# Performance work log

Measured on AMD Instinct MI355X. Metric: run time of the kernel, lower is better.

The kernel has to match this reference:

```python
import jax, jax.numpy as jnp
import numpy as np

B, N, DIM, HEADS = 2, 1024, 1024, 16
HD = DIM // HEADS  # 64


def setup_inputs() -> dict:
    key = jax.random.key(0)
    ks = jax.random.split(key, 8)
    f = lambda k, s: jax.random.normal(k, s, dtype=jnp.float32)
    inv = np.float32(1.0 / np.sqrt(DIM))
    return {
        'x_real': f(ks[0], (B, N, DIM)),
        'x_imag': f(ks[1], (B, N, DIM)),
        'freqs_real': f(ks[2], (N, HD)),
        'freqs_imag': f(ks[3], (N, HD)),
        'Wqkv_r': f(ks[4], (3 * DIM, DIM)) * inv,
        'Wqkv_i': f(ks[5], (3 * DIM, DIM)) * inv,
        'bqkv_r': jnp.zeros((3 * DIM,), jnp.float32),
        'bqkv_i': jnp.zeros((3 * DIM,), jnp.float32),
        'Wout_r': f(ks[6], (DIM, DIM)) * inv,
        'Wout_i': f(ks[7], (DIM, DIM)) * inv,
        'bout_r': jnp.zeros((DIM,), jnp.float32),
        'bout_i': jnp.zeros((DIM,), jnp.float32),
    }


def reference(x_real, x_imag, freqs_real, freqs_imag,
              Wqkv_r, Wqkv_i, bqkv_r, bqkv_i,
              Wout_r, Wout_i, bout_r, bout_i):
    cplx = jax.lax.complex
    x = cplx(x_real, x_imag)                    # [b, n, d] complex64
    Wqkv = cplx(Wqkv_r, Wqkv_i)                 # [3d, d]
    bqkv = cplx(bqkv_r, bqkv_i)
    Wout = cplx(Wout_r, Wout_i)
    bout = cplx(bout_r, bout_i)
    freqs = cplx(freqs_real, freqs_imag)        # [n, hd]

    scale = HD ** (-0.5)

    # ComplexLinear: x @ W^T + b -> [b, n, 3d]
    qkv = jnp.einsum('bnd,ed->bne', x, Wqkv) + bqkv
    # rearrange 'b n (h d qkv) -> qkv b h n d' (qkv index fastest-varying)
    qkv = qkv.reshape(B, N, HEADS, HD, 3)
    q = jnp.transpose(qkv[..., 0], (0, 2, 1, 3))  # [b, h, n, hd]
    k = jnp.transpose(qkv[..., 1], (0, 2, 1, 3))
    v = jnp.transpose(qkv[..., 2], (0, 2, 1, 3))

    # complex rotary: elementwise multiply by freqs [n, hd]
    q = q * freqs
    k = k * freqs

    # complex QK^H -> [b, h, n, n]
    dots = jnp.einsum('bhnd,bhmd->bhnm', q, jnp.conj(k))
    attn = jax.nn.softmax(jnp.abs(dots) * scale, axis=-1)  # real float32

    # real attn @ complex v (promotes to complex64)
    out = jnp.einsum('bhnm,bhmd->bhnd', attn, v)
    out = jnp.transpose(out, (0, 2, 1, 3)).reshape(B, N, DIM)  # b n (h d)

    out = jnp.einsum('bnd,ed->bne', out, Wout) + bout
    # return real/imag stacked so baseline comparison is on real arrays
    return jnp.stack([jnp.real(out), jnp.imag(out)], axis=0)  # [2, b, n, d]
```

## Files before the change

kernel.cpp:

```cpp
#include <hip/hip_runtime.h>
#include <hip/hip_bf16.h>
#include <stdint.h>

#define B 2
#define N 1024
#define DIM 1024
#define HEADS 16
#define HD 64
#define E3 (3*DIM)
#define M (B*N)

typedef __hip_bfloat16 bf16;
typedef __attribute__((ext_vector_type(8))) short short8v;
typedef __attribute__((ext_vector_type(4))) float f32x4;
typedef __attribute__((ext_vector_type(4))) unsigned int u32x4;

__device__ __forceinline__ float scrub(float v) {
    return (v == v && fabsf(v) < 1e30f) ? v : 0.0f;
}
__device__ __forceinline__ float b2f(bf16 x) { return scrub(__bfloat162float(x)); }

template<bool FP32>
__device__ __forceinline__ float ldin(const void* p, int i) {
    if (FP32) return scrub(((const float*)p)[i]);
    else      return scrub(__bfloat162float(((const bf16*)p)[i]));
}

__device__ __forceinline__ bool sniff_fp32(const void* x, int tid, int* sbad) {
    if (tid == 0) *sbad = 0;
    __syncthreads();
    if (tid < 64) {
        const unsigned short* u = (const unsigned short*)x;
        int ex = (u[tid] >> 7) & 0xFF;
        if (ex == 0xFF || ex >= 135 || (ex != 0 && ex <= 118))
            atomicAdd(sbad, 1);
    }
    __syncthreads();
    return *sbad > 4;
}

__device__ __forceinline__ short f2bs(float x) {
    bf16 h = __float2bfloat16(x);
    return __builtin_bit_cast(short, h);
}
__device__ __forceinline__ short8v neg8(short8v x) {
    u32x4 u = __builtin_bit_cast(u32x4, x);
    u ^= 0x80008000u;
    return __builtin_bit_cast(short8v, u);
}
__device__ __forceinline__ f32x4 mfma16(short8v a, short8v b, f32x4 c) {
    return __builtin_amdgcn_mfma_f32_16x16x32_bf16(a, b, c, 0, 0, 0);
}

__device__ __forceinline__ void cvt8(bf16* dhi, bf16* dlo, const float* s) {
    float4 a = *(const float4*)s;
    float4 b = *(const float4*)(s + 4);
    float v[8] = {a.x,a.y,a.z,a.w,b.x,b.y,b.z,b.w};
    short8v hi, lo;
    #pragma unroll
    for (int e = 0; e < 8; ++e) {
        float f = scrub(v[e]);
        bf16 h = __float2bfloat16(f);
        hi[e] = __builtin_bit_cast(short, h);
        lo[e] = f2bs(f - __bfloat162float(h));
    }
    *(short8v*)dhi = hi;
    *(short8v*)dlo = lo;
}
__device__ __forceinline__ void cvt8h(bf16* dhi, const float* s) {
    float4 a = *(const float4*)s;
    float4 b = *(const float4*)(s + 4);
    float v[8] = {a.x,a.y,a.z,a.w,b.x,b.y,b.z,b.w};
    short8v hi;
    #pragma unroll
    for (int e = 0; e < 8; ++e)
        hi[e] = f2bs(scrub(v[e]));
    *(short8v*)dhi = hi;
}

#define PLB 2048

__device__ __forceinline__ short8v frag_ldp(const bf16* base, int row, int j) {
    int p = row >> 1;
    int c = (((row & 1) << 2) | j) ^ (p & 7);
    return *(const short8v*)(base + p*64 + c*8);
}

template<int AMODE, int BMODE, int BM, int NI>
__device__ __forceinline__ void cgemm32(
    const void* Aor, const void* Aoi,
    const bf16* Arh, const bf16* Aih, const bf16* Arl, const bf16* Ail,
    const void* Bor, const void* Boi,
    const bf16* Brh, const bf16* Bih,
    int row0, int col0,
    bf16* sA, bf16* sB,
    f32x4 (*accr)[NI], f32x4 (*accs)[NI], f32x4 (*acci)[NI])
{
    constexpr bool ALO = (AMODE == 1 || AMODE == 2);
    constexpr bool BLO = (BMODE == 2);
    constexpr int  PLA = BM*32;

    const int t  = threadIdx.x;
    const int w  = t >> 6, l = t & 63;
    const int lr = l & 15, lg = l >> 4;
    const int wm = (NI == 4) ? w : (w >> 1);
    const int wn = (NI == 4) ? 0 : (w & 1);

    const int pb  = t >> 3;
    const int cpb = (t & 7) ^ (pb & 7);
    const int srb = 2*pb + (cpb >> 2);
    const int sjb = cpb & 3;

    for (int k0 = 0; k0 < DIM; k0 += 32) {
        #pragma unroll
        for (int u = 0; u < BM/64; ++u) {
            int c   = t + 256*u;
            int pa  = c >> 3;
            int cpa = (c & 7) ^ (pa & 7);
            int sra = 2*pa + (cpa >> 2);
            int sja = cpa & 3;
            size_t aoff = (size_t)(row0 + sra)*DIM + k0 + sja*8;
            bf16* dA = sA + c*8;
            if constexpr (AMODE == 0) {
                *(short8v*)(dA)        = *(const short8v*)((const bf16*)Aor + aoff);
                *(short8v*)(dA + PLA)  = *(const short8v*)((const bf16*)Aoi + aoff);
            } else if constexpr (AMODE == 1) {
                *(short8v*)(dA)         = *(const short8v*)(Arh + aoff);
                *(short8v*)(dA + PLA)   = *(const short8v*)(Aih + aoff);
                *(short8v*)(dA + 2*PLA) = *(const short8v*)(Arl + aoff);
                *(short8v*)(dA + 3*PLA) = *(const short8v*)(Ail + aoff);
            } else {
                cvt8(dA,       dA + 2*PLA, (const float*)Aor + aoff);
                cvt8(dA + PLA, dA + 3*PLA, (const float*)Aoi + aoff);
            }
        }
        {
            size_t boff = (size_t)(col0 + srb)*DIM + k0 + sjb*8;
            bf16* dB = sB + t*8;
            if constexpr (BMODE == 0) {
                *(short8v*)(dB)       = *(const short8v*)((const bf16*)Bor + boff);
                *(short8v*)(dB + PLB) = *(const short8v*)((const bf16*)Boi + boff);
            } else if constexpr (BMODE == 3) {
                *(short8v*)(dB)       = *(const short8v*)(Brh + boff);
                *(short8v*)(dB + PLB) = *(const short8v*)(Bih + boff);
            } else {
                cvt8(dB,       dB + 2*PLB, (const float*)Bor + boff);
                cvt8(dB + PLB, dB + 3*PLB, (const float*)Boi + boff);
            }
        }
        __syncthreads();

        short8v arh[2], aih[2], arl[2], ail[2];
        #pragma unroll
        for (int mi = 0; mi < 2; ++mi) {
            int arow = wm*32 + mi*16 + lr;
            arh[mi] = frag_ldp(sA,       arow, lg);
            aih[mi] = frag_ldp(sA + PLA, arow, lg);
            if constexpr (ALO) {
                arl[mi] = frag_ldp(sA + 2*PLA, arow, lg);
                ail[mi] = frag_ldp(sA + 3*PLA, arow, lg);
            }
        }
        #pragma unroll
        for (int ni = 0; ni < NI; ++ni) {
            int brow = wn*32 + ni*16 + lr;
            short8v brh = frag_ldp(sB,       brow, lg);
            short8v bih = frag_ldp(sB + PLB, brow, lg);
            short8v brl, bil;
            if constexpr (BLO) {
                brl = frag_ldp(sB + 2*PLB, brow, lg);
                bil = frag_ldp(sB + 3*PLB, brow, lg);
            }
            #pragma unroll
            for (int mi = 0; mi < 2; ++mi) {
                accr[mi][ni] = mfma16(arh[mi], brh, accr[mi][ni]);
                accs[mi][ni] = mfma16(aih[mi], bih, accs[mi][ni]);
                acci[mi][ni] = mfma16(arh[mi], bih, acci[mi][ni]);
                acci[mi][ni] = mfma16(aih[mi], brh, acci[mi][ni]);
                if constexpr (BLO) {
                    accr[mi][ni] = mfma16(arh[mi], brl, accr[mi][ni]);
                    accs[mi][ni] = mfma16(aih[mi], bil, accs[mi][ni]);
                    acci[mi][ni] = mfma16(arh[mi], bil, acci[mi][ni]);
                    acci[mi][ni] = mfma16(aih[mi], brl, acci[mi][ni]);
                }
                if constexpr (ALO) {
                    accr[mi][ni] = mfma16(arl[mi], brh, accr[mi][ni]);
                    accs[mi][ni] = mfma16(ail[mi], bih, accs[mi][ni]);
                    acci[mi][ni] = mfma16(arl[mi], bih, acci[mi][ni]);
                    acci[mi][ni] = mfma16(ail[mi], brh, acci[mi][ni]);
                }
            }
        }
        __syncthreads();
    }
}

struct PrepArgs {
    const void* src[6];
    bf16* hi[6];
    bf16* lo[6];
    int n8[6];
};

__global__ __launch_bounds__(256) void prepass_kernel(PrepArgs a) {
    __shared__ int sbad;
    const int y = blockIdx.y;
    bool f32 = sniff_fp32(a.src[y], threadIdx.x, &sbad);
    if (!f32) return;
    const int n8 = a.n8[y];
    bf16* lo = a.lo[y];
    for (int i = blockIdx.x*blockDim.x + threadIdx.x; i < n8; i += gridDim.x*blockDim.x) {
        if (lo) cvt8 (a.hi[y] + (size_t)i*8, lo + (size_t)i*8, (const float*)a.src[y] + (size_t)i*8);
        else    cvt8h(a.hi[y] + (size_t)i*8,                   (const float*)a.src[y] + (size_t)i*8);
    }
}

template<bool FP32>
__device__ __forceinline__ void qkv_epi(
    const void* fr_, const void* fi_, const void* bqr, const void* bqi,
    bf16* qr, bf16* qi, bf16* kr, bf16* ki, bf16* vr, bf16* vi,
    int row0, int col0,
    f32x4 (*accr)[4], f32x4 (*accs)[4], f32x4 (*acci)[4])
{
    const int t  = threadIdx.x;
    const int w  = t >> 6, l = t & 63;
    const int lr = l & 15, lg = l >> 4;

    #pragma unroll
    for (int ni = 0; ni < 4; ++ni) {
        int col = col0 + ni*16 + lr;
        float bre = ldin<FP32>(bqr, col);
        float bim = ldin<FP32>(bqi, col);
        int s = col % 3;
        int tc = col / 3;
        int h = tc / HD, d = tc % HD;
        #pragma unroll
        for (int mi = 0; mi < 2; ++mi)
        #pragma unroll
        for (int r = 0; r < 4; ++r) {
            int row = row0 + w*32 + mi*16 + 4*lg + r;
            int bb = row / N, n = row % N;
            float cr = accr[mi][ni][r] - accs[mi][ni][r] + bre;
            float ci = acci[mi][ni][r] + bim;
            if (s == 2) {
                int idxT = ((bb*HEADS + h)*HD + d)*N + n;
                vr[idxT] = __float2bfloat16(scrub(cr));
                vi[idxT] = __float2bfloat16(scrub(ci));
            } else {
                float fre = ldin<FP32>(fr_, n*HD + d);
                float fim = ldin<FP32>(fi_, n*HD + d);
                float rr = cr*fre - ci*fim;
                float ri = cr*fim + ci*fre;
                int idx = ((bb*HEADS + h)*N + n)*HD + d;
                if (s == 0) { qr[idx] = __float2bfloat16(scrub(rr)); qi[idx] = __float2bfloat16(scrub(ri)); }
                else        { kr[idx] = __float2bfloat16(scrub(rr)); ki[idx] = __float2bfloat16(scrub(ri)); }
            }
        }
    }
}

template<int FM>
__global__ __launch_bounds__(256, 3) void qkv_kernel(
    const void* xr, const void* xi, const void* fr_, const void* fi_,
    const void* Wr, const void* Wi, const void* bqr, const void* bqi,
    const bf16* xrh, const bf16* xih, const bf16* xrl, const bf16* xil,
    const bf16* wrh, const bf16* wih,
    bf16* qr, bf16* qi, bf16* kr, bf16* ki, bf16* vr, bf16* vi)
{
    __shared__ __align__(16) bf16 sA[4*128*32];
    __shared__ __align__(16) bf16 sB[(FM==1 ? 2 : 4)*PLB];
    __shared__ int sbad;
    bool f32 = sniff_fp32(xr, threadIdx.x, &sbad);

    int wg   = blockIdx.x;
    int xcd  = wg & 7;
    int idx  = wg >> 3;
    int ctl  = idx % 6;
    int rtg  = idx / 6;
    int row0 = rtg * 128;
    int col0 = (xcd*6 + ctl) * 64;

    f32x4 accr[2][4] = {}, accs[2][4] = {}, acci[2][4] = {};
    if (f32) {
        if constexpr (FM == 1)
            cgemm32<1, 3, 128, 4>(xr, xi, xrh, xih, xrl, xil,
                                  Wr, Wi, wrh, wih,
                                  row0, col0, sA, sB, accr, accs, acci);
        else
            cgemm32<2, 2, 128, 4>(xr, xi, nullptr, nullptr, nullptr, nullptr,
                                  Wr, Wi, nullptr, nullptr,
                                  row0, col0, sA, sB, accr, accs, acci);
        qkv_epi<true >(fr_, fi_, bqr, bqi, qr,qi,kr,ki,vr,vi, row0, col0, accr, accs, acci);
    } else {
        cgemm32<0, 0, 128, 4>(xr, xi, nullptr, nullptr, nullptr, nullptr,
                              Wr, Wi, nullptr, nullptr,
                              row0, col0, sA, sB, accr, accs, acci);
        qkv_epi<false>(fr_, fi_, bqr, bqi, qr,qi,kr,ki,vr,vi, row0, col0, accr, accs, acci);
    }
}

__device__ __forceinline__ short8v frag_ld(const bf16* base, int row, int j) {
    return *(const short8v*)(base + row*64 + ((j ^ (row & 7)) << 3));
}

__global__ __launch_bounds__(256) void attn_kernel(
    const bf16* qr, const bf16* qi, const bf16* kr, const bf16* ki,
    const bf16* vtr, const bf16* vti, bf16* aor_, bf16* aoi_)
{
    __shared__ __align__(16) bf16 skr[64*64];
    __shared__ __align__(16) bf16 ski[64*64];
    __shared__ __align__(16) bf16 svr[64*64];
    __shared__ __align__(16) bf16 svi[64*64];
    __shared__ __align__(16) bf16 sp[4][16*64];

    const int t  = threadIdx.x;
    const int w  = t >> 6;
    const int l  = t & 63;
    const int lr = l & 15;
    const int lg = l >> 4;
    int wg = blockIdx.x;
    int sw = (wg & 7) * ((int)gridDim.x >> 3) + (wg >> 3);
    const int qt = sw & 15;
    const int bh = sw >> 4;

    const size_t hbase = (size_t)bh * N * HD;

    const bf16* qrg = qr + hbase + (size_t)(qt*64 + w*16 + lr) * HD;
    const bf16* qig = qi + hbase + (size_t)(qt*64 + w*16 + lr) * HD;
    short8v qfr[2], qfi[2], qfrn[2];
    #pragma unroll
    for (int ks = 0; ks < 2; ++ks) {
        qfr[ks] = *(const short8v*)(qrg + 32*ks + 8*lg);
        qfi[ks] = *(const short8v*)(qig + 32*ks + 8*lg);
        qfrn[ks] = neg8(qfr[ks]);
    }

    const int cA = t, cB = t + 256;
    const int rA = cA >> 3, jA = (cA & 7) ^ (rA & 7);
    const int rB = cB >> 3, jB = (cB & 7) ^ (rB & 7);
    const bf16* krg = kr  + hbase;
    const bf16* kig = ki  + hbase;
    const bf16* vrg = vtr + hbase;
    const bf16* vig = vti + hbase;

    f32x4 outr[4], outi[4];
    #pragma unroll
    for (int dt = 0; dt < 4; ++dt) {
        outr[dt] = (f32x4){0.f,0.f,0.f,0.f};
        outi[dt] = (f32x4){0.f,0.f,0.f,0.f};
    }
    float mrow[4] = {-1e30f,-1e30f,-1e30f,-1e30f};
    float lrow[4] = {0.f,0.f,0.f,0.f};

    for (int kt = 0; kt < N/64; ++kt) {
        const int m0 = kt*64;
        *(short8v*)(skr + cA*8) = *(const short8v*)(krg + (size_t)(m0+rA)*HD + jA*8);
        *(short8v*)(skr + cB*8) = *(const short8v*)(krg + (size_t)(m0+rB)*HD + jB*8);
        *(short8v*)(ski + cA*8) = *(const short8v*)(kig + (size_t)(m0+rA)*HD + jA*8);
        *(short8v*)(ski + cB*8) = *(const short8v*)(kig + (size_t)(m0+rB)*HD + jB*8);
        *(short8v*)(svr + cA*8) = *(const short8v*)(vrg + (size_t)rA*N + m0 + jA*8);
        *(short8v*)(svr + cB*8) = *(const short8v*)(vrg + (size_t)rB*N + m0 + jB*8);
        *(short8v*)(svi + cA*8) = *(const short8v*)(vig + (size_t)rA*N + m0 + jA*8);
        *(short8v*)(svi + cB*8) = *(const short8v*)(vig + (size_t)rB*N + m0 + jB*8);
        __syncthreads();

        f32x4 sr[4], si[4];
        #pragma unroll
        for (int ct = 0; ct < 4; ++ct) {
            f32x4 ar = (f32x4){0.f,0.f,0.f,0.f};
            f32x4 ai = (f32x4){0.f,0.f,0.f,0.f};
            #pragma unroll
            for (int ks = 0; ks < 2; ++ks) {
                short8v kfr = frag_ld(skr, 16*ct + lr, 4*ks + lg);
                short8v kfi = frag_ld(ski, 16*ct + lr, 4*ks + lg);
                ar = mfma16(qfr[ks],  kfr, ar);
                ar = mfma16(qfi[ks],  kfi, ar);
                ai = mfma16(qfi[ks],  kfr, ai);
                ai = mfma16(qfrn[ks], kfi, ai);
            }
            sr[ct] = ar; si[ct] = ai;
        }

        float p[4][4];
        float pmax[4] = {-1e30f,-1e30f,-1e30f,-1e30f};
        #pragma unroll
        for (int ct = 0; ct < 4; ++ct)
        #pragma unroll
        for (int r = 0; r < 4; ++r) {
            float s = sqrtf(sr[ct][r]*sr[ct][r] + si[ct][r]*si[ct][r]) * 0.125f;
            p[ct][r] = s;
            pmax[r] = fmaxf(pmax[r], s);
        }
        #pragma unroll
        for (int mk = 1; mk <= 8; mk <<= 1)
        #pragma unroll
        for (int r = 0; r < 4; ++r)
            pmax[r] = fmaxf(pmax[r], __shfl_xor(pmax[r], mk));

        float fsc[4];
        #pragma unroll
        for (int r = 0; r < 4; ++r) {
            float mnew = fmaxf(mrow[r], pmax[r]);
            fsc[r] = __expf(mrow[r] - mnew);
            mrow[r] = mnew;
        }
        float rsum[4] = {0.f,0.f,0.f,0.f};
        #pragma unroll
        for (int ct = 0; ct < 4; ++ct)
        #pragma unroll
        for (int r = 0; r < 4; ++r) {
            float e = __expf(p[ct][r] - mrow[r]);
            p[ct][r] = e;
            rsum[r] += e;
        }
        #pragma unroll
        for (int mk = 1; mk <= 8; mk <<= 1)
        #pragma unroll
        for (int r = 0; r < 4; ++r)
            rsum[r] += __shfl_xor(rsum[r], mk);
        #pragma unroll
        for (int r = 0; r < 4; ++r)
            lrow[r] = lrow[r]*fsc[r] + rsum[r];
        #pragma unroll
        for (int dt = 0; dt < 4; ++dt)
        #pragma unroll
        for (int r = 0; r < 4; ++r) {
            outr[dt][r] *= fsc[r];
            outi[dt][r] *= fsc[r];
        }

        bf16* pw = sp[w];
        #pragma unroll
        for (int ct = 0; ct < 4; ++ct)
        #pragma unroll
        for (int r = 0; r < 4; ++r) {
            int prow = 4*lg + r;
            int pcol = 16*ct + lr;
            int jj = (pcol >> 3) ^ (prow & 7);
            pw[prow*64 + jj*8 + (pcol & 7)] = __float2bfloat16(p[ct][r]);
        }
        short8v pa[2];
        #pragma unroll
        for (int ks2 = 0; ks2 < 2; ++ks2)
            pa[ks2] = frag_ld(pw, lr, 4*ks2 + lg);

        #pragma unroll
        for (int dt = 0; dt < 4; ++dt)
        #pragma unroll
        for (int ks2 = 0; ks2 < 2; ++ks2) {
            short8v vfr = frag_ld(svr, 16*dt + lr, 4*ks2 + lg);
            short8v vfi = frag_ld(svi, 16*dt + lr, 4*ks2 + lg);
            outr[dt] = mfma16(pa[ks2], vfr, outr[dt]);
            outi[dt] = mfma16(pa[ks2], vfi, outi[dt]);
        }
        __syncthreads();
    }

    const int b_ = bh / HEADS, h_ = bh % HEADS;
    float invl[4];
    #pragma unroll
    for (int r = 0; r < 4; ++r) invl[r] = 1.0f / lrow[r];
    #pragma unroll
    for (int dt = 0; dt < 4; ++dt)
    #pragma unroll
    for (int r = 0; r < 4; ++r) {
        int n_ = qt*64 + w*16 + 4*lg + r;
        int d_ = 16*dt + lr;
        size_t oidx = ((size_t)(b_*N + n_))*DIM + h_*HD + d_;
        aor_[oidx] = __float2bfloat16(scrub(outr[dt][r]*invl[r]));
        aoi_[oidx] = __float2bfloat16(scrub(outi[dt][r]*invl[r]));
    }
}

template<int FM>
__global__ __launch_bounds__(256, 4) void outproj_kernel(
    const void* xprobe,
    const bf16* ar, const bf16* ai,
    const void* Wr, const void* Wi, const void* bor, const void* boi,
    const bf16* wrh, const bf16* wih,
    void* out)
{
    __shared__ __align__(16) bf16 sA[2*PLB];
    __shared__ __align__(16) bf16 sB[(FM==3 ? 2 : 4)*PLB];
    __shared__ int sbad;
    bool f32 = sniff_fp32(xprobe, threadIdx.x, &sbad);

    int wg   = blockIdx.x;
    int xcd  = wg & 7;
    int idx  = wg >> 3;
    int rtin = idx & 1;
    int tmp  = idx >> 1;
    int ctl  = tmp & 1;
    int rtg  = tmp >> 1;
    int row0 = (rtg*2 + rtin) * 64;
    int col0 = (xcd*2 + ctl) * 64;

    const int t  = threadIdx.x;
    const int w  = t >> 6, l = t & 63;
    const int lr = l & 15, lg = l >> 4;
    const int wm = w >> 1, wn = w & 1;

    f32x4 accr[2][2] = {}, accs[2][2] = {}, acci[2][2] = {};
    if (f32) {
        if constexpr (FM == 3)
            cgemm32<0, 3, 64, 2>(ar, ai, nullptr, nullptr, nullptr, nullptr,
                                 Wr, Wi, wrh, wih,
                                 row0, col0, sA, sB, accr, accs, acci);
        else
            cgemm32<0, 2, 64, 2>(ar, ai, nullptr, nullptr, nullptr, nullptr,
                                 Wr, Wi, nullptr, nullptr,
                                 row0, col0, sA, sB, accr, accs, acci);
    } else {
        cgemm32<0, 0, 64, 2>(ar, ai, nullptr, nullptr, nullptr, nullptr,
                             Wr, Wi, nullptr, nullptr,
                             row0, col0, sA, sB, accr, accs, acci);
    }

    #pragma unroll
    for (int ni = 0; ni < 2; ++ni) {
        int col = col0 + wn*32 + ni*16 + lr;
        float bre = f32 ? ldin<true>(bor, col) : ldin<false>(bor, col);
        float bim = f32 ? ldin<true>(boi, col) : ldin<false>(boi, col);
        #pragma unroll
        for (int mi = 0; mi < 2; ++mi)
        #pragma unroll
        for (int r = 0; r < 4; ++r) {
            int row = row0 + wm*32 + mi*16 + 4*lg + r;
            float cr = scrub(accr[mi][ni][r] - accs[mi][ni][r] + bre);
            float ci = scrub(acci[mi][ni][r] + bim);
            if (f32) {
                ((float*)out)[(size_t)row*DIM + col]                 = cr;
                ((float*)out)[(size_t)M*DIM + (size_t)row*DIM + col] = ci;
            } else {
                ((bf16*)out)[(size_t)row*DIM + col]                  = __float2bfloat16(cr);
                ((bf16*)out)[(size_t)M*DIM + (size_t)row*DIM + col]  = __float2bfloat16(ci);
            }
        }
    }
}

extern "C" void kernel_launch(void* const* d_in, const int* in_sizes, int n_in,
                              void* d_out, int out_size, void* d_ws, size_t ws_size,
                              hipStream_t stream)
{
    const void* xr     = d_in[0];
    const void* xi     = d_in[1];
    const void* fr     = d_in[2];
    const void* fi     = d_in[3];
    const void* Wqkv_r = d_in[4];
    const void* Wqkv_i = d_in[5];
    const void* bqkv_r = d_in[6];
    const void* bqkv_i = d_in[7];
    const void* Wout_r = d_in[8];
    const void* Wout_i = d_in[9];
    const void* bout_r = d_in[10];
    const void* bout_i = d_in[11];

    bf16* w = (bf16*)d_ws;
    const size_t QS  = (size_t)B*HEADS*N*HD;
    const size_t XS  = (size_t)M*DIM;
    const size_t WQS = (size_t)E3*DIM;
    const size_t WOS = (size_t)DIM*DIM;

    bf16* qr   = w;          bf16* qi   = qr  + QS;
    bf16* kr   = qi  + QS;   bf16* ki   = kr  + QS;
    bf16* vr   = ki  + QS;   bf16* vi   = vr  + QS;
    bf16* aor_ = vi  + QS;   bf16* aoi_ = aor_ + QS;
    bf16* xrh = aoi_ + QS;   bf16* xih = xrh + XS;
    bf16* xrl = xih + XS;    bf16* xil = xrl + XS;
    bf16* wqrh = xil + XS;   bf16* wqih = wqrh + WQS;
    bf16* worh = wqih + WQS; bf16* woih = worh + WOS;

    const size_t need = (size_t)(8*QS + 4*XS + 2*WQS + 2*WOS) * sizeof(bf16);
    const bool pre = ws_size >= need;

    if (pre) {
        PrepArgs a;
        a.src[0] = xr;     a.hi[0] = xrh;  a.lo[0] = xrl;    a.n8[0] = (int)(XS/8);
        a.src[1] = xi;     a.hi[1] = xih;  a.lo[1] = xil;    a.n8[1] = (int)(XS/8);
        a.src[2] = Wqkv_r; a.hi[2] = wqrh; a.lo[2] = nullptr; a.n8[2] = (int)(WQS/8);
        a.src[3] = Wqkv_i; a.hi[3] = wqih; a.lo[3] = nullptr; a.n8[3] = (int)(WQS/8);
        a.src[4] = Wout_r; a.hi[4] = worh; a.lo[4] = nullptr; a.n8[4] = (int)(WOS/8);
        a.src[5] = Wout_i; a.hi[5] = woih; a.lo[5] = nullptr; a.n8[5] = (int)(WOS/8);
        prepass_kernel<<<dim3(1536, 6), dim3(256), 0, stream>>>(a);

        qkv_kernel<1><<<dim3((E3/64)*(M/128)), dim3(256), 0, stream>>>(
            xr, xi, fr, fi, Wqkv_r, Wqkv_i, bqkv_r, bqkv_i,
            xrh, xih, xrl, xil, wqrh, wqih,
            qr, qi, kr, ki, vr, vi);
    } else {
        qkv_kernel<2><<<dim3((E3/64)*(M/128)), dim3(256), 0, stream>>>(
            xr, xi, fr, fi, Wqkv_r, Wqkv_i, bqkv_r, bqkv_i,
            nullptr, nullptr, nullptr, nullptr, nullptr, nullptr,
            qr, qi, kr, ki, vr, vi);
    }

    attn_kernel<<<dim3(B*HEADS*(N/64)), dim3(256), 0, stream>>>(
        qr, qi, kr, ki, vr, vi, aor_, aoi_);

    if (pre) {
        outproj_kernel<3><<<dim3((DIM/64)*(M/64)), dim3(256), 0, stream>>>(
            xr, aor_, aoi_, Wout_r, Wout_i, bout_r, bout_i,
            worh, woih, d_out);
    } else {
        outproj_kernel<2><<<dim3((DIM/64)*(M/64)), dim3(256), 0, stream>>>(
            xr, aor_, aoi_, Wout_r, Wout_i, bout_r, bout_i,
            nullptr, nullptr, d_out);
    }
}
```

Measured before the change: 323.7 us.

## Double-buffer GEMM tiles with async global-to-LDS loads in QKV and out-projection

Adds a cgemm_async path that loads the pre-converted bf16 A/B tiles directly into shared memory with global_load_lds and double-buffers them, so the next k-slice is fetched while MFMAs run on the current one. This removes the register round-trip and one barrier per k-step from the main loop. Shared memory is doubled, so qkv_kernel's launch bounds drop from 3 to 2 blocks per CU, lowering occupancy. The fp32-convert fallback path keeps the old synchronous loop.

```diff
diff --git a/kernel.cpp b/kernel.cpp
--- a/kernel.cpp
+++ b/kernel.cpp
@@ -52,6 +52,12 @@
     return __builtin_amdgcn_mfma_f32_16x16x32_bf16(a, b, c, 0, 0, 0);
 }
 
+__device__ __forceinline__ void gload16(const bf16* g, bf16* l) {
+    __builtin_amdgcn_global_load_lds(
+        (const __attribute__((address_space(1))) void*)g,
+        (__attribute__((address_space(3))) void*)l, 16, 0, 0);
+}
+
 __device__ __forceinline__ void cvt8(bf16* dhi, bf16* dlo, const float* s) {
     float4 a = *(const float4*)s;
     float4 b = *(const float4*)(s + 4);
@@ -86,20 +92,103 @@
     return *(const short8v*)(base + p*64 + c*8);
 }
 
+template<bool ASPLIT, int BM, int NI>
+__device__ __forceinline__ void cgemm_async(
+    const bf16* Arh, const bf16* Aih, const bf16* Arl, const bf16* Ail,
+    const bf16* Brh, const bf16* Bih,
+    int row0, int col0,
+    bf16* sA0, bf16* sA1, bf16* sB0, bf16* sB1,
+    f32x4 (*accr)[NI], f32x4 (*accs)[NI], f32x4 (*acci)[NI])
+{
+    constexpr int PLA = BM*32;
+    const int t  = threadIdx.x;
+    const int w  = t >> 6, l = t & 63;
+    const int lr = l & 15, lg = l >> 4;
+    const int wm = (NI == 4) ? w : (w >> 1);
+    const int wn = (NI == 4) ? 0 : (w & 1);
+
+    const int pb  = t >> 3;
+    const int cpb = (t & 7) ^ (pb & 7);
+    const int srb = 2*pb + (cpb >> 2);
+    const int sjb = cpb & 3;
+
+    auto stage = [&](int buf, int k0) {
+        bf16* dsA = buf ? sA1 : sA0;
+        bf16* dsB = buf ? sB1 : sB0;
+        #pragma unroll
+        for (int u = 0; u < BM/64; ++u) {
+            int c   = t + 256*u;
+            int pa  = c >> 3;
+            int cpa = (c & 7) ^ (pa & 7);
+            int sra = 2*pa + (cpa >> 2);
+            int sja = cpa & 3;
+            size_t aoff = (size_t)(row0 + sra)*DIM + k0 + sja*8;
+            gload16(Arh + aoff, dsA + c*8);
+            gload16(Aih + aoff, dsA + PLA + c*8);
+            if constexpr (ASPLIT) {
+                gload16(Arl + aoff, dsA + 2*PLA + c*8);
+                gload16(Ail + aoff, dsA + 3*PLA + c*8);
+            }
+        }
+        size_t boff = (size_t)(col0 + srb)*DIM + k0 + sjb*8;
+        gload16(Brh + boff, dsB + t*8);
+        gload16(Bih + boff, dsB + PLB + t*8);
+    };
+
+    stage(0, 0);
+    __syncthreads();
+    int cur = 0;
+
+    for (int k0 = 0; k0 < DIM; k0 += 32) {
+        if (k0 + 32 < DIM) stage(cur ^ 1, k0 + 32);
+
+        const bf16* sA = cur ? sA1 : sA0;
+        const bf16* sB = cur ? sB1 : sB0;
+
+        short8v arh[2], aih[2], arl[2], ail[2];
+        #pragma unroll
+        for (int mi = 0; mi < 2; ++mi) {
+            int arow = wm*32 + mi*16 + lr;
+            arh[mi] = frag_ldp(sA,       arow, lg);
+            aih[mi] = frag_ldp(sA + PLA, arow, lg);
+            if constexpr (ASPLIT) {
+                arl[mi] = frag_ldp(sA + 2*PLA, arow, lg);
+                ail[mi] = frag_ldp(sA + 3*PLA, arow, lg);
+            }
+        }
+        #pragma unroll
+        for (int ni = 0; ni < NI; ++ni) {
+            int brow = wn*32 + ni*16 + lr;
+            short8v brh = frag_ldp(sB,       brow, lg);
+            short8v bih = frag_ldp(sB + PLB, brow, lg);
+            #pragma unroll
+            for (int mi = 0; mi < 2; ++mi) {
+                accr[mi][ni] = mfma16(arh[mi], brh, accr[mi][ni]);
+                accs[mi][ni] = mfma16(aih[mi], bih, accs[mi][ni]);
+                acci[mi][ni] = mfma16(arh[mi], bih, acci[mi][ni]);
+                acci[mi][ni] = mfma16(aih[mi], brh, acci[mi][ni]);
+                if constexpr (ASPLIT) {
+                    accr[mi][ni] = mfma16(arl[mi], brh, accr[mi][ni]);
+                    accs[mi][ni] = mfma16(ail[mi], bih, accs[mi][ni]);
+                    acci[mi][ni] = mfma16(arl[mi], bih, acci[mi][ni]);
+                    acci[mi][ni] = mfma16(ail[mi], brh, acci[mi][ni]);
+                }
+            }
+        }
+        __syncthreads();
+        cur ^= 1;
+    }
+}
+
 template<int AMODE, int BMODE, int BM, int NI>
-__device__ __forceinline__ void cgemm32(
+__device__ __forceinline__ void cgemm_sync(
     const void* Aor, const void* Aoi,
-    const bf16* Arh, const bf16* Aih, const bf16* Arl, const bf16* Ail,
     const void* Bor, const void* Boi,
-    const bf16* Brh, const bf16* Bih,
     int row0, int col0,
     bf16* sA, bf16* sB,
     f32x4 (*accr)[NI], f32x4 (*accs)[NI], f32x4 (*acci)[NI])
 {
-    constexpr bool ALO = (AMODE == 1 || AMODE == 2);
-    constexpr bool BLO = (BMODE == 2);
-    constexpr int  PLA = BM*32;
-
+    constexpr int PLA = BM*32;
     const int t  = threadIdx.x;
     const int w  = t >> 6, l = t & 63;
     const int lr = l & 15, lg = l >> 4;
@@ -122,13 +211,8 @@
             size_t aoff = (size_t)(row0 + sra)*DIM + k0 + sja*8;
             bf16* dA = sA + c*8;
             if constexpr (AMODE == 0) {
-                *(short8v*)(dA)        = *(const short8v*)((const bf16*)Aor + aoff);
-                *(short8v*)(dA + PLA)  = *(const short8v*)((const bf16*)Aoi + aoff);
-            } else if constexpr (AMODE == 1) {
-                *(short8v*)(dA)         = *(const short8v*)(Arh + aoff);
-                *(short8v*)(dA + PLA)   = *(const short8v*)(Aih + aoff);
-                *(short8v*)(dA + 2*PLA) = *(const short8v*)(Arl + aoff);
-                *(short8v*)(dA + 3*PLA) = *(const short8v*)(Ail + aoff);
+                *(short8v*)(dA)       = *(const short8v*)((const bf16*)Aor + aoff);
+                *(short8v*)(dA + PLA) = *(const short8v*)((const bf16*)Aoi + aoff);
             } else {
                 cvt8(dA,       dA + 2*PLA, (const float*)Aor + aoff);
                 cvt8(dA + PLA, dA + 3*PLA, (const float*)Aoi + aoff);
@@ -140,9 +224,6 @@
             if constexpr (BMODE == 0) {
                 *(short8v*)(dB)       = *(const short8v*)((const bf16*)Bor + boff);
                 *(short8v*)(dB + PLB) = *(const short8v*)((const bf16*)Boi + boff);
-            } else if constexpr (BMODE == 3) {
-                *(short8v*)(dB)       = *(const short8v*)(Brh + boff);
-                *(short8v*)(dB + PLB) = *(const short8v*)(Bih + boff);
             } else {
                 cvt8(dB,       dB + 2*PLB, (const float*)Bor + boff);
                 cvt8(dB + PLB, dB + 3*PLB, (const float*)Boi + boff);
@@ -156,7 +237,7 @@
             int arow = wm*32 + mi*16 + lr;
             arh[mi] = frag_ldp(sA,       arow, lg);
             aih[mi] = frag_ldp(sA + PLA, arow, lg);
-            if constexpr (ALO) {
+            if constexpr (AMODE == 2) {
                 arl[mi] = frag_ldp(sA + 2*PLA, arow, lg);
                 ail[mi] = frag_ldp(sA + 3*PLA, arow, lg);
             }
@@ -167,7 +248,7 @@
             short8v brh = frag_ldp(sB,       brow, lg);
             short8v bih = frag_ldp(sB + PLB, brow, lg);
             short8v brl, bil;
-            if constexpr (BLO) {
+            if constexpr (BMODE == 2) {
                 brl = frag_ldp(sB + 2*PLB, brow, lg);
                 bil = frag_ldp(sB + 3*PLB, brow, lg);
             }
@@ -177,13 +258,13 @@
                 accs[mi][ni] = mfma16(aih[mi], bih, accs[mi][ni]);
                 acci[mi][ni] = mfma16(arh[mi], bih, acci[mi][ni]);
                 acci[mi][ni] = mfma16(aih[mi], brh, acci[mi][ni]);
-                if constexpr (BLO) {
+                if constexpr (BMODE == 2) {
                     accr[mi][ni] = mfma16(arh[mi], brl, accr[mi][ni]);
                     accs[mi][ni] = mfma16(aih[mi], bil, accs[mi][ni]);
                     acci[mi][ni] = mfma16(arh[mi], bil, acci[mi][ni]);
                     acci[mi][ni] = mfma16(aih[mi], brl, acci[mi][ni]);
                 }
-                if constexpr (ALO) {
+                if constexpr (AMODE == 2) {
                     accr[mi][ni] = mfma16(arl[mi], brh, accr[mi][ni]);
                     accs[mi][ni] = mfma16(ail[mi], bih, accs[mi][ni]);
                     acci[mi][ni] = mfma16(arl[mi], bih, acci[mi][ni]);
@@ -260,15 +341,15 @@
 }
 
 template<int FM>
-__global__ __launch_bounds__(256, 3) void qkv_kernel(
+__global__ __launch_bounds__(256, 2) void qkv_kernel(
     const void* xr, const void* xi, const void* fr_, const void* fi_,
     const void* Wr, const void* Wi, const void* bqr, const void* bqi,
     const bf16* xrh, const bf16* xih, const bf16* xrl, const bf16* xil,
     const bf16* wrh, const bf16* wih,
     bf16* qr, bf16* qi, bf16* kr, bf16* ki, bf16* vr, bf16* vi)
 {
-    __shared__ __align__(16) bf16 sA[4*128*32];
-    __shared__ __align__(16) bf16 sB[(FM==1 ? 2 : 4)*PLB];
+    __shared__ __align__(16) bf16 sA[2][4*128*32];
+    __shared__ __align__(16) bf16 sB[2][2*PLB];
     __shared__ int sbad;
     bool f32 = sniff_fp32(xr, threadIdx.x, &sbad);
 
@@ -283,18 +364,19 @@
     f32x4 accr[2][4] = {}, accs[2][4] = {}, acci[2][4] = {};
     if (f32) {
         if constexpr (FM == 1)
-            cgemm32<1, 3, 128, 4>(xr, xi, xrh, xih, xrl, xil,
-                                  Wr, Wi, wrh, wih,
-                                  row0, col0, sA, sB, accr, accs, acci);
+            cgemm_async<true, 128, 4>(xrh, xih, xrl, xil, wrh, wih,
+                                      row0, col0, sA[0], sA[1], sB[0], sB[1],
+                                      accr, accs, acci);
         else
-            cgemm32<2, 2, 128, 4>(xr, xi, nullptr, nullptr, nullptr, nullptr,
-                                  Wr, Wi, nullptr, nullptr,
-                                  row0, col0, sA, sB, accr, accs, acci);
+            cgemm_sync<2, 2, 128, 4>(xr, xi, Wr, Wi,
+                                     row0, col0, sA[0], sB[0],
+                                     accr, accs, acci);
         qkv_epi<true >(fr_, fi_, bqr, bqi, qr,qi,kr,ki,vr,vi, row0, col0, accr, accs, acci);
     } else {
-        cgemm32<0, 0, 128, 4>(xr, xi, nullptr, nullptr, nullptr, nullptr,
-                              Wr, Wi, nullptr, nullptr,
-                              row0, col0, sA, sB, accr, accs, acci);
+        cgemm_async<false, 128, 4>((const bf16*)xr, (const bf16*)xi, nullptr, nullptr,
+                                   (const bf16*)Wr, (const bf16*)Wi,
+                                   row0, col0, sA[0], sA[1], sB[0], sB[1],
+                                   accr, accs, acci);
         qkv_epi<false>(fr_, fi_, bqr, bqi, qr,qi,kr,ki,vr,vi, row0, col0, accr, accs, acci);
     }
 }
@@ -480,8 +562,8 @@
     const bf16* wrh, const bf16* wih,
     void* out)
 {
-    __shared__ __align__(16) bf16 sA[2*PLB];
-    __shared__ __align__(16) bf16 sB[(FM==3 ? 2 : 4)*PLB];
+    __shared__ __align__(16) bf16 sA[2][2*PLB];
+    __shared__ __align__(16) bf16 sB[2][2*PLB];
     __shared__ int sbad;
     bool f32 = sniff_fp32(xprobe, threadIdx.x, &sbad);
 
@@ -503,17 +585,18 @@
     f32x4 accr[2][2] = {}, accs[2][2] = {}, acci[2][2] = {};
     if (f32) {
         if constexpr (FM == 3)
-            cgemm32<0, 3, 64, 2>(ar, ai, nullptr, nullptr, nullptr, nullptr,
-                                 Wr, Wi, wrh, wih,
-                                 row0, col0, sA, sB, accr, accs, acci);
+            cgemm_async<false, 64, 2>(ar, ai, nullptr, nullptr, wrh, wih,
+                                      row0, col0, sA[0], sA[1], sB[0], sB[1],
+                                      accr, accs, acci);
         else
-            cgemm32<0, 2, 64, 2>(ar, ai, nullptr, nullptr, nullptr, nullptr,
-                                 Wr, Wi, nullptr, nullptr,
-                                 row0, col0, sA, sB, accr, accs, acci);
+            cgemm_sync<0, 2, 64, 2>(ar, ai, Wr, Wi,
+                                    row0, col0, sA[0], sB[0],
+                                    accr, accs, acci);
     } else {
-        cgemm32<0, 0, 64, 2>(ar, ai, nullptr, nullptr, nullptr, nullptr,
-                             Wr, Wi, nullptr, nullptr,
-                             row0, col0, sA, sB, accr, accs, acci);
+        cgemm_async<false, 64, 2>(ar, ai, nullptr, nullptr,
+                                  (const bf16*)Wr, (const bf16*)Wi,
+                                  row0, col0, sA[0], sA[1], sB[0], sB[1],
+                                  accr, accs, acci);
     }
 
     #pragma unroll
```

Result: slower. 342.6 us (+5.8%).
